# Kernel tuning notes

Measured on AMD Instinct MI355X. Metric: run time of the kernel, lower is better.

The kernel has to match this reference:

```python
import jax, jax.numpy as jnp
import numpy as np

jax.config.update("jax_enable_x64", True)

N_USERS = 100000
N_ITEMS = 50000
N = N_USERS + N_ITEMS          # total nodes
E = 4_000_000                  # nnz of adj
MASK_DEPTH = 2
KEEP_RATE = 0.1
N_SEEDS = 500


def setup_inputs() -> dict:
    key = jax.random.key(0)
    k1, k2, k3, k4 = jax.random.split(key, 4)
    rows = jax.random.randint(k1, (E,), 0, N, dtype=jnp.int64)
    cols = jax.random.randint(k2, (E,), 0, N, dtype=jnp.int64)
    seeds = jax.random.randint(k3, (N_SEEDS,), 0, N, dtype=jnp.int64)
    adj_vals = jax.random.uniform(k4, (E,), dtype=jnp.float32)
    return {"adj_vals": adj_vals, "rows": rows, "cols": cols, "seeds": seeds}


def _mask_subgraphs(adj_vals, rows, cols, seeds, key):
    # --- vectorized BFS-style edge masking (equivalent to the serial per-seed
    # loop: the set of removed edges per depth is the union over the frontier,
    # and collected endpoints are identical to the sequential version) ---
    alive = jnp.ones(E, dtype=bool)                    # edges not yet masked
    frontier = jnp.zeros(N, dtype=bool).at[seeds].set(True)
    masked_nodes = frontier                            # maskNodes accumulator
    for i in range(MASK_DEPTH):
        idct = (frontier[rows] | frontier[cols]) & alive
        alive = alive & ~idct
        if i != MASK_DEPTH - 1:
            hits = (jnp.zeros(N, jnp.int32)
                    .at[rows].add(idct.astype(jnp.int32))
                    .at[cols].add(idct.astype(jnp.int32)))
            frontier = hits > 0                        # unique(concat(nxtSeeds))
            masked_nodes = masked_nodes | frontier
    # random augmentation of the masked node set
    samp_num = int(N * KEEP_RATE)
    ks, kr, kc = jax.random.split(key, 3)
    sampled = jax.random.randint(ks, (samp_num,), 0, N)
    masked_nodes = masked_nodes.at[sampled].set(True)

    # --- encoderAdj: remaining edges with value 1, symmetric degree norm ---
    alive_f = alive.astype(jnp.float32)
    deg = jnp.zeros(N, jnp.float32).at[rows].add(alive_f)   # sparse row sum
    dnorm = jnp.power(deg + 1e-12, -0.5)
    enc_vals = alive_f * dnorm[rows] * dnorm[cols]          # 0 for masked edges

    # --- decoderAdj: random edges among masked nodes + self loops + remaining
    # edges, dedup'd through the row*N+col hash ---
    order = jnp.argsort(~masked_nodes)        # masked node ids first, ascending
    tem_num = masked_nodes.sum()
    i1 = jnp.minimum((jax.random.uniform(kr, (E,)) * tem_num).astype(jnp.int64),
                     tem_num - 1)
    i2 = jnp.minimum((jax.random.uniform(kc, (E,)) * tem_num).astype(jnp.int64),
                     tem_num - 1)
    tr = order[i1]
    tc = order[i2]
    ar = jnp.arange(N, dtype=jnp.int64)
    # masked (dead) edges collapse onto the (0,0) self-loop hash so the
    # fixed-size unique removes them, mirroring the compaction in torch
    h_tail = jnp.where(alive, rows * N + cols, 0)
    hashv = jnp.concatenate([tr * N + tc, tc * N + tr, ar * (N + 1), h_tail])
    uniq = jnp.unique(hashv, size=hashv.shape[0], fill_value=-1)
    valid = uniq >= 0
    dec_vals = valid.astype(jnp.float32)
    dec_cols = jnp.where(valid, uniq % N, 0)
    dec_rows = jnp.where(valid, uniq // N, 0)
    return rows, cols, enc_vals, dec_rows, dec_cols, dec_vals


def reference(adj_vals, rows, cols, seeds):
    key = jax.random.key(42)
    # returns (encoder indices+values, decoder indices+values); padded decoder
    # slots carry value 0 (equivalent sparse matrix)
    return _mask_subgraphs(adj_vals, rows, cols, seeds, key)
```

## Files before the change

### kernel.cpp

```cpp
#include <hip/hip_runtime.h>
#include <stdint.h>

#define NNODE   150000
#define EDGES   4000000
#define NSEED   500
#define NSAMP   15000
#define MOUT    12150000
#define SENTK   0xFFFFFFFFFFFFFFFFULL
#define SPAN    150000ULL
#define MULTK   51616ULL
#define FIXED   8150000

#define CHUNK   8192
#define TH      512
#define NC      1488
#define NCX     (NC / 8)
#define MP      ((size_t)NC * CHUNK)
#define RADIX   512
#define NHIST   (RADIX * NC)
#define SCB     (NHIST / 2048)
#define NTILE   NC

#define EBLK    2048
#define ENB     ((EDGES + EBLK - 1) / EBLK)

#define MTILE   2048
#define MB      ((NNODE + MTILE - 1) / MTILE)

#define OUT_DR  12000000
#define OUT_DC  24150000
#define OUT_DV  36300000

__host__ __device__ inline void tf2x32(uint32_t k0, uint32_t k1,
                                       uint32_t x0, uint32_t x1,
                                       uint32_t& o0, uint32_t& o1) {
  uint32_t ks2 = k0 ^ k1 ^ 0x1BD11BDAu;
  x0 += k0; x1 += k1;
#define TFR(d) { x0 += x1; x1 = (x1 << d) | (x1 >> (32 - d)); x1 ^= x0; }
  TFR(13) TFR(15) TFR(26) TFR(6)
  x0 += k1; x1 += ks2 + 1u;
  TFR(17) TFR(29) TFR(16) TFR(24)
  x0 += ks2; x1 += k0 + 2u;
  TFR(13) TFR(15) TFR(26) TFR(6)
  x0 += k0; x1 += k1 + 3u;
  TFR(17) TFR(29) TFR(16) TFR(24)
  x0 += k1; x1 += ks2 + 4u;
  TFR(13) TFR(15) TFR(26) TFR(6)
  x0 += ks2; x1 += k0 + 5u;
#undef TFR
  o0 = x0; o1 = x1;
}

__device__ inline unsigned long long tf_bits64(uint32_t k0, uint32_t k1, uint32_t i) {
  uint32_t o0, o1;
  tf2x32(k0, k1, 0u, i, o0, o1);
  return ((unsigned long long)o0 << 32) | o1;
}

__device__ inline int activeChunks(const int* counters) {
  int m2 = FIXED + counters[2];
  return (m2 + CHUNK - 1) / CHUNK;
}

__device__ inline int block_excl_scan_256(int v, int* lds , int& total) {
  int lane = threadIdx.x & 63, wid = threadIdx.x >> 6;
  int inc = v;
#pragma unroll
  for (int off = 1; off < 64; off <<= 1) {
    int y = __shfl_up(inc, off, 64);
    if (lane >= off) inc += y;
  }
  if (lane == 63) lds[wid] = inc;
  __syncthreads();
  if (threadIdx.x == 0) {
    int a = 0;
#pragma unroll
    for (int w = 0; w < 4; ++w) { int t = lds[w]; lds[w] = a; a += t; }
    lds[4] = a;
  }
  __syncthreads();
  total = lds[4];
  int res = inc - v + lds[wid];
  __syncthreads();
  return res;
}

__device__ inline void scan512_x4(const int v[4], int ex[4], int tot[4], int* aux) {
  int lane = threadIdx.x & 63, wid = threadIdx.x >> 6;
  int inc[4];
#pragma unroll
  for (int j = 0; j < 4; ++j) inc[j] = v[j];
#pragma unroll
  for (int off = 1; off < 64; off <<= 1) {
#pragma unroll
    for (int j = 0; j < 4; ++j) {
      int y = __shfl_up(inc[j], off, 64);
      if (lane >= off) inc[j] += y;
    }
  }
  if (lane == 63) {
#pragma unroll
    for (int j = 0; j < 4; ++j) aux[j * 8 + wid] = inc[j];
  }
  __syncthreads();
  if (threadIdx.x == 0) {
#pragma unroll
    for (int j = 0; j < 4; ++j) {
      int a = 0;
#pragma unroll
      for (int w = 0; w < 8; ++w) { int t = aux[j * 8 + w]; aux[j * 8 + w] = a; a += t; }
      aux[32 + j] = a;
    }
  }
  __syncthreads();
#pragma unroll
  for (int j = 0; j < 4; ++j) {
    ex[j] = inc[j] - v[j] + aux[j * 8 + wid];
    tot[j] = aux[32 + j];
  }
}

__device__ inline int scan512_1(int v, int* aux ) {
  int lane = threadIdx.x & 63, wid = threadIdx.x >> 6;
  int inc = v;
#pragma unroll
  for (int off = 1; off < 64; off <<= 1) {
    int y = __shfl_up(inc, off, 64);
    if (lane >= off) inc += y;
  }
  if (lane == 63) aux[wid] = inc;
  __syncthreads();
  if (threadIdx.x == 0) {
    int a = 0;
#pragma unroll
    for (int w = 0; w < 8; ++w) { int t = aux[w]; aux[w] = a; a += t; }
  }
  __syncthreads();
  return inc - v + aux[wid];
}

__device__ inline int phys16(int p) { return (p & ~15) | ((p + (p >> 4)) & 15); }

__global__ __launch_bounds__(256) void k_seed(const int* seeds, uint8_t* frontier, uint8_t* masked) {
  int i = blockIdx.x * 256 + threadIdx.x;
  if (i < NSEED) { int v = seeds[i]; frontier[v] = 1; masked[v] = 1; }
}

__global__ __launch_bounds__(256) void k_bfs0(const int* rows, const int* cols,
                                              const uint8_t* frontier, uint8_t* alive, uint8_t* nxt,
                                              float* out) {
  int e = blockIdx.x * 256 + threadIdx.x;
  int r = rows[e], c = cols[e];
  out[e] = (float)r;
  out[EDGES + e] = (float)c;
  if (frontier[r] | frontier[c]) { alive[e] = 0; nxt[r] = 1; nxt[c] = 1; }
}

__global__ __launch_bounds__(256) void k_masked_or(uint8_t* masked, const uint8_t* nxt) {
  int v = blockIdx.x * 256 + threadIdx.x;
  if (v < NNODE) masked[v] |= nxt[v];
}

__global__ __launch_bounds__(256) void k_bfs1deg(const int* rows, const int* cols,
                                                 const uint8_t* nxt, uint8_t* alive, float* deg) {
  int e = blockIdx.x * 256 + threadIdx.x;
  int r = rows[e];
  int a = alive[e];
  if (a && (nxt[r] | nxt[cols[e]])) { alive[e] = 0; a = 0; }
  if (a) atomicAdd(&deg[r], 1.0f);
}

__global__ __launch_bounds__(256) void k_sample(uint8_t* masked,
                                                uint32_t a0, uint32_t a1, uint32_t b0, uint32_t b1) {
  int i = blockIdx.x * 256 + threadIdx.x;
  if (i >= NSAMP) return;
  unsigned long long hi = tf_bits64(a0, a1, (uint32_t)i);
  unsigned long long lo = tf_bits64(b0, b1, (uint32_t)i);
  unsigned long long off = ((hi % SPAN) * MULTK + (lo % SPAN)) % SPAN;
  masked[off] = 1;
}

__global__ __launch_bounds__(256) void k_dnorm(const float* deg, float* dnorm) {
  int v = blockIdx.x * 256 + threadIdx.x;
  if (v < NNODE) {
    float x = deg[v] + 1e-12f;
    dnorm[v] = (float)(1.0 / sqrt((double)x));
  }
}

__global__ __launch_bounds__(256) void k_enctail(const int* rows, const int* cols,
                                                 const uint8_t* alive, const float* dnorm,
                                                 float* out, unsigned long long* A, int* counters) {
  __shared__ int lds[8];
  __shared__ unsigned long long stage[EBLK];
  __shared__ int sbase;
  int base = blockIdx.x * EBLK;
  unsigned long long vv[8];
  int emit[8], c = 0;
#pragma unroll
  for (int k = 0; k < 8; ++k) {
    int e = base + k * 256 + threadIdx.x;
    emit[k] = 0;
    if (e < EDGES) {
      int r = rows[e], cc = cols[e];
      int a = alive[e];
      out[2 * EDGES + e] = a ? dnorm[r] * dnorm[cc] : 0.0f;
      unsigned long long v = (unsigned long long)((long long)r * 150000LL + cc);
      if (a && v) { emit[k] = 1; vv[k] = v; c++; }
    }
  }
  int total;
  int ex = block_excl_scan_256(c, lds, total);
#pragma unroll
  for (int k = 0; k < 8; ++k) {
    if (emit[k]) stage[ex++] = vv[k];
  }
  if (threadIdx.x == 0) sbase = total ? atomicAdd(&counters[2], total) : 0;
  __syncthreads();
  int sb = sbase;
  for (int i = threadIdx.x; i < total; i += 256)
    A[(size_t)FIXED + sb + i] = stage[i];
}

__global__ __launch_bounds__(256) void k_mreduce(const uint8_t* masked, int* mPart) {
  __shared__ int lds[4];
  int base = blockIdx.x * MTILE;
  int s = 0;
  for (int i = threadIdx.x; i < MTILE; i += 256) {
    int idx = base + i;
    if (idx < NNODE) s += masked[idx];
  }
#pragma unroll
  for (int off = 32; off; off >>= 1) s += __shfl_down(s, off, 64);
  if ((threadIdx.x & 63) == 0) lds[threadIdx.x >> 6] = s;
  __syncthreads();
  if (threadIdx.x == 0) mPart[blockIdx.x] = lds[0] + lds[1] + lds[2] + lds[3];
}

__global__ __launch_bounds__(1024) void k_scan_small(int* part, int m, int* totalOut) {
  __shared__ int a[2048];
  int tid = threadIdx.x;
  a[tid] = (tid < m) ? part[tid] : 0;
  a[tid + 1024] = (tid + 1024 < m) ? part[tid + 1024] : 0;
  __syncthreads();
  for (int off = 1; off < 2048; off <<= 1) {
    int v1 = 0, v2;
    if (tid >= off) v1 = a[tid - off];
    v2 = a[tid + 1024 - off];
    __syncthreads();
    if (tid >= off) a[tid] += v1;
    a[tid + 1024] += v2;
    __syncthreads();
  }
  if (tid < m) part[tid] = (tid == 0) ? 0 : a[tid - 1];
  if (tid + 1024 < m) part[tid + 1024] = a[tid + 1023];
  if (tid == 0 && totalOut) *totalOut = a[2047];
}

__global__ __launch_bounds__(256) void k_mscatter(const uint8_t* masked, const int* mPart, int* mlist) {
  __shared__ int lds[8];
  int t0 = blockIdx.x * MTILE + threadIdx.x * 8;
  int c = 0;
#pragma unroll
  for (int k = 0; k < 8; ++k) { int idx = t0 + k; c += (idx < NNODE) ? masked[idx] : 0; }
  int total;
  int ex = block_excl_scan_256(c, lds, total);
  int run = mPart[blockIdx.x] + ex;
#pragma unroll
  for (int k = 0; k < 8; ++k) {
    int idx = t0 + k;
    if (idx < NNODE && masked[idx]) mlist[run++] = idx;
  }
}

__global__ __launch_bounds__(256) void k_build_pairs(const int* mlist, const int* counters,
                                                     unsigned long long* A,
                                                     uint32_t r0, uint32_t r1, uint32_t c0, uint32_t c1) {
  int e = blockIdx.x * 256 + threadIdx.x;
  long long tem = counters[1];
  unsigned long long bits = tf_bits64(r0, r1, (uint32_t)e);
  double u1 = __longlong_as_double((long long)((bits >> 12) | 0x3FF0000000000000ULL)) - 1.0;
  long long i1 = (long long)(u1 * (double)tem); if (i1 > tem - 1) i1 = tem - 1;
  bits = tf_bits64(c0, c1, (uint32_t)e);
  double u2 = __longlong_as_double((long long)((bits >> 12) | 0x3FF0000000000000ULL)) - 1.0;
  long long i2 = (long long)(u2 * (double)tem); if (i2 > tem - 1) i2 = tem - 1;
  long long tr = mlist[i1], tc = mlist[i2];
  A[2 * (size_t)e]     = (unsigned long long)(tr * 150000LL + tc);
  A[2 * (size_t)e + 1] = (unsigned long long)(tc * 150000LL + tr);
}

__global__ __launch_bounds__(256) void k_build_self(unsigned long long* A) {
  int v = blockIdx.x * 256 + threadIdx.x;
  if (v >= NNODE) return;
  A[2 * (size_t)EDGES + v] = (unsigned long long)v * 150001ULL;
}

__global__ __launch_bounds__(256) void k_pad(unsigned long long* A, const int* counters) {
  int m2 = FIXED + counters[2];
  int ac = (m2 + CHUNK - 1) / CHUNK;
  size_t idx = (size_t)m2 + blockIdx.x * 256 + threadIdx.x;
  if (idx < (size_t)ac * CHUNK) A[idx] = SENTK;
}

__global__ __launch_bounds__(TH) void k_rhist2(const unsigned long long* __restrict__ src,
                                               int* __restrict__ hist, int shift,
                                               const int* counters) {
  __shared__ int h8[RADIX * 4];
  int tid = threadIdx.x;
  int ac = activeChunks(counters);
  if ((int)blockIdx.x >= ac) { hist[(size_t)tid * NC + blockIdx.x] = 0; return; }
  for (int i = tid; i < RADIX * 4; i += TH) h8[i] = 0;
  __syncthreads();
  const ulonglong2* s2 = (const ulonglong2*)(src + (size_t)blockIdx.x * CHUNK);
  int rep = tid & 3, scnt = 0;
#pragma unroll
  for (int r = 0; r < 8; ++r) {
    ulonglong2 v = s2[tid + r * TH];
    int d0 = (int)((v.x >> shift) & (RADIX - 1));
    int d1 = (int)((v.y >> shift) & (RADIX - 1));
    if (d0 == RADIX - 1) scnt++; else atomicAdd(&h8[d0 * 4 + rep], 1);
    if (d1 == RADIX - 1) scnt++; else atomicAdd(&h8[d1 * 4 + rep], 1);
  }
  if (scnt) atomicAdd(&h8[(RADIX - 1) * 4 + rep], scnt);
  __syncthreads();
  int4 hv = *(const int4*)&h8[tid * 4];
  hist[(size_t)tid * NC + blockIdx.x] = hv.x + hv.y + hv.z + hv.w;
}

__global__ __launch_bounds__(256) void k_scan_reduce(const int* g, int* part, int n) {
  __shared__ int lds[4];
  int base = blockIdx.x * 2048;
  int s = 0;
  for (int i = threadIdx.x; i < 2048; i += 256) {
    int idx = base + i;
    if (idx < n) s += g[idx];
  }
#pragma unroll
  for (int off = 32; off; off >>= 1) s += __shfl_down(s, off, 64);
  if ((threadIdx.x & 63) == 0) lds[threadIdx.x >> 6] = s;
  __syncthreads();
  if (threadIdx.x == 0) part[blockIdx.x] = lds[0] + lds[1] + lds[2] + lds[3];
}

__global__ __launch_bounds__(256) void k_scan_apply(int* g, const int* part, int n) {
  __shared__ int lds[8];
  int t0 = blockIdx.x * 2048 + threadIdx.x * 8;
  int x[8];
#pragma unroll
  for (int k = 0; k < 8; ++k) { int idx = t0 + k; x[k] = (idx < n) ? g[idx] : 0; }
  int s = 0;
#pragma unroll
  for (int k = 0; k < 8; ++k) { int t = x[k]; x[k] = s; s += t; }
  int total;
  int ex = block_excl_scan_256(s, lds, total);
  int add = part[blockIdx.x] + ex;
#pragma unroll
  for (int k = 0; k < 8; ++k) { int idx = t0 + k; if (idx < n) g[idx] = x[k] + add; }
}

__global__ __launch_bounds__(TH) void k_rscatter2(const unsigned long long* __restrict__ src,
                                                  unsigned long long* __restrict__ dst,
                                                  const int* __restrict__ hist, int shift,
                                                  const int* counters) {
  __shared__ uint32_t klo[CHUNK], khi[CHUNK];
  __shared__ int h8[RADIX * 4];
  __shared__ int dstart[RADIX], gbase[RADIX];
  __shared__ int aux[40];
  int tid = threadIdx.x;
  int chunk = (blockIdx.x & 7) * NCX + (blockIdx.x >> 3);
  int ac = activeChunks(counters);
  if (chunk >= ac) return;
  size_t cbase = (size_t)chunk * CHUNK;
  gbase[tid] = hist[(size_t)tid * NC + chunk];
  for (int i = tid; i < RADIX * 4; i += TH) h8[i] = 0;
  __syncthreads();
  int rep = tid & 3;
  const ulonglong2* s2 = (const ulonglong2*)(src + cbase);
  int scnt = 0;
#pragma unroll
  for (int r = 0; r < 8; ++r) {
    ulonglong2 v = s2[tid + r * TH];
    int i = 2 * (tid + r * TH);
    int p0 = phys16(i), p1 = phys16(i + 1);
    klo[p0] = (uint32_t)v.x; khi[p0] = (uint32_t)(v.x >> 32);
    klo[p1] = (uint32_t)v.y; khi[p1] = (uint32_t)(v.y >> 32);
    int d0 = (int)((v.x >> shift) & (RADIX - 1));
    int d1 = (int)((v.y >> shift) & (RADIX - 1));
    if (d0 == RADIX - 1) scnt++; else atomicAdd(&h8[d0 * 4 + rep], 1);
    if (d1 == RADIX - 1) scnt++; else atomicAdd(&h8[d1 * 4 + rep], 1);
  }
  if (scnt) atomicAdd(&h8[(RADIX - 1) * 4 + rep], scnt);
  __syncthreads();
  int4 hv = *(const int4*)&h8[tid * 4];
  int h = hv.x + hv.y + hv.z + hv.w;
  int ex0 = scan512_1(h, aux);
  dstart[tid] = ex0;
  __syncthreads();
  int t0 = tid * 16;
  for (int rr = 0; rr < 3; ++rr) {
    int sh = shift + 3 * rr;
    unsigned long long key[16];
    unsigned long long cpack = 0;
#pragma unroll
    for (int k = 0; k < 16; ++k) {
      int p = phys16(t0 + k);
      key[k] = ((unsigned long long)khi[p] << 32) | klo[p];
      cpack += 1ULL << (((int)(key[k] >> sh) & 7) << 3);
    }
    int v4[4], ex[4], tot[4];
#pragma unroll
    for (int j = 0; j < 4; ++j) {
      unsigned pair = (unsigned)(cpack >> (16 * j));
      v4[j] = (int)((pair & 0xffu) | ((pair & 0xff00u) << 8));
    }
    scan512_x4(v4, ex, tot, aux);
    unsigned long long startq0, startq1;
    {
      int a = 0, s8[8];
#pragma unroll
      for (int j = 0; j < 4; ++j) {
        int tlo = tot[j] & 0xffff, thi = tot[j] >> 16;
        int elo = ex[j] & 0xffff,  ehi = ex[j] >> 16;
        s8[2 * j]     = a + elo; a += tlo;
        s8[2 * j + 1] = a + ehi; a += thi;
      }
      startq0 = (unsigned long long)(unsigned)s8[0]
              | ((unsigned long long)(unsigned)s8[1] << 16)
              | ((unsigned long long)(unsigned)s8[2] << 32)
              | ((unsigned long long)(unsigned)s8[3] << 48);
      startq1 = (unsigned long long)(unsigned)s8[4]
              | ((unsigned long long)(unsigned)s8[5] << 16)
              | ((unsigned long long)(unsigned)s8[6] << 32)
              | ((unsigned long long)(unsigned)s8[7] << 48);
    }
#pragma unroll
    for (int k = 0; k < 16; ++k) {
      int d = (int)(key[k] >> sh) & 7;
      int fs = (d & 3) << 4;
      unsigned long long inc = 1ULL << fs;
      int pos;
      if (d < 4) { pos = (int)((startq0 >> fs) & 0xffffu); startq0 += inc; }
      else       { pos = (int)((startq1 >> fs) & 0xffffu); startq1 += inc; }
      int p = phys16(pos);
      klo[p] = (uint32_t)key[k]; khi[p] = (uint32_t)(key[k] >> 32);
    }
    __syncthreads();
  }
#pragma unroll
  for (int r = 0; r < 16; ++r) {
    int i = tid + r * TH;
    int p = phys16(i);
    unsigned long long k1 = ((unsigned long long)khi[p] << 32) | klo[p];
    int d = (int)((k1 >> shift) & (RADIX - 1));
    dst[(size_t)(gbase[d] + (i - dstart[d]))] = k1;
  }
}

__global__ __launch_bounds__(TH) void k_uniq_count(const unsigned long long* A, int* uPart,
                                                   const int* counters) {
  __shared__ int lds[8];
  int ac = activeChunks(counters);
  if ((int)blockIdx.x >= ac) { if (threadIdx.x == 0) uPart[blockIdx.x] = 0; return; }
  size_t base = (size_t)blockIdx.x * CHUNK + (size_t)threadIdx.x * 16;
  unsigned long long prev = (base == 0) ? 0ULL : A[base - 1];
  int c = 0;
#pragma unroll
  for (int k = 0; k < 16; ++k) {
    unsigned long long v = A[base + k];
    c += (v != SENTK && v != prev) ? 1 : 0;
    prev = v;
  }
#pragma unroll
  for (int off = 32; off; off >>= 1) c += __shfl_down(c, off, 64);
  if ((threadIdx.x & 63) == 0) lds[threadIdx.x >> 6] = c;
  __syncthreads();
  if (threadIdx.x == 0) {
    int s = 0;
#pragma unroll
    for (int w = 0; w < 8; ++w) s += lds[w];
    uPart[blockIdx.x] = s;
  }
}

__global__ __launch_bounds__(TH) void k_final(const unsigned long long* A, const int* uPart,
                                              const int* counters, float* out) {
  __shared__ int aux[9];
  __shared__ float sq[CHUNK], sr[CHUNK];
  __shared__ int scnt;
  int ac = activeChunks(counters);
  if ((int)blockIdx.x >= ac) return;
  size_t base = (size_t)blockIdx.x * CHUNK + (size_t)threadIdx.x * 16;
  unsigned long long v[16];
  int f[16], c = 0;
  unsigned long long prev = (base == 0) ? 0ULL : A[base - 1];
#pragma unroll
  for (int k = 0; k < 16; ++k) {
    v[k] = A[base + k];
    f[k] = (v[k] != SENTK && v[k] != prev) ? 1 : 0;
    c += f[k];
    prev = v[k];
  }
  int ex = scan512_1(c, aux);
  if (threadIdx.x == TH - 1) scnt = ex + c;
  int j = ex;
#pragma unroll
  for (int k = 0; k < 16; ++k) {
    if (f[k]) {
      unsigned long long val = v[k];
      long long q = (long long)((double)val * (1.0 / 150000.0));
      long long r = (long long)val - q * 150000LL;
      if (r < 0) { q--; r += 150000LL; }
      else if (r >= 150000LL) { q++; r -= 150000LL; }
      sq[j] = (float)q; sr[j] = (float)r; j++;
    }
  }
  __syncthreads();
  int cnt = scnt;
  int jb = 1 + uPart[blockIdx.x];
  for (int i = (int)threadIdx.x; i < cnt; i += TH) {
    out[OUT_DR + jb + i] = sq[i];
    out[OUT_DC + jb + i] = sr[i];
  }
}

__global__ __launch_bounds__(256) void k_dectail(const int* counters, float* out) {
  int i = (blockIdx.x * 256 + threadIdx.x) * 4;
  if (i >= MOUT) return;
  int totU = counters[3] + 1;
  float4 dv;
  dv.x = (i + 0 < totU) ? 1.0f : 0.0f;
  dv.y = (i + 1 < totU) ? 1.0f : 0.0f;
  dv.z = (i + 2 < totU) ? 1.0f : 0.0f;
  dv.w = (i + 3 < totU) ? 1.0f : 0.0f;
  *(float4*)&out[OUT_DV + i] = dv;
  if (i + 3 >= totU) {
    float4 z = make_float4(0.0f, 0.0f, 0.0f, 0.0f);
    if (i >= totU) {
      *(float4*)&out[OUT_DR + i] = z;
      *(float4*)&out[OUT_DC + i] = z;
    } else {
#pragma unroll
      for (int k = 0; k < 4; ++k)
        if (i + k >= totU) { out[OUT_DR + i + k] = 0.0f; out[OUT_DC + i + k] = 0.0f; }
    }
  }
  if (i == 0) { out[OUT_DR] = 0.0f; out[OUT_DC] = 0.0f; }
}

extern "C" void kernel_launch(void* const* d_in, const int* in_sizes, int n_in,
                              void* d_out, int out_size, void* d_ws, size_t ws_size,
                              hipStream_t stream) {
  const int* rows = (const int*)d_in[1];
  const int* cols = (const int*)d_in[2];
  const int* seeds = (const int*)d_in[3];
  float* out = (float*)d_out;

  char* ws = (char*)d_ws;
  size_t off = 0;
  auto alloc = [&](size_t bytes) -> char* {
    char* p = ws + off;
    off += (bytes + 255) & ~(size_t)255;
    return p;
  };
  unsigned long long* A = (unsigned long long*)alloc(MP * 8);
  uint8_t* alive = (uint8_t*)alloc(EDGES);
  char* zbase = ws + off;
  uint8_t* frontier = (uint8_t*)alloc(NNODE);
  uint8_t* nextf = (uint8_t*)alloc(NNODE);
  uint8_t* masked = (uint8_t*)alloc(NNODE);
  float* deg = (float*)alloc((size_t)NNODE * 4);
  int* counters = (int*)alloc(256 * 4);
  size_t zsize = (size_t)((ws + off) - zbase);
  float* dnorm = (float*)alloc((size_t)NNODE * 4);
  int* mlist = (int*)alloc((size_t)NNODE * 4);
  int* hist = (int*)alloc((size_t)NHIST * 4);
  int* spart = (int*)alloc(2048 * 4);
  int* uPart = (int*)alloc(2048 * 4);
  int* mPart = (int*)alloc(256 * 4);

  unsigned long long* Bbuf = (unsigned long long*)(out + OUT_DR);

  uint32_t ks0, ks1, kr0, kr1, kc0, kc1, s10, s11, s20, s21;
  tf2x32(0u, 42u, 0u, 0u, ks0, ks1);
  tf2x32(0u, 42u, 0u, 1u, kr0, kr1);
  tf2x32(0u, 42u, 0u, 2u, kc0, kc1);
  tf2x32(ks0, ks1, 0u, 0u, s10, s11);
  tf2x32(ks0, ks1, 0u, 1u, s20, s21);

  hipMemsetAsync(zbase, 0, zsize, stream);
  hipMemsetAsync(alive, 1, EDGES, stream);

  const int EB = EDGES / 256;
  const int NB = (NNODE + 255) / 256;

  k_seed<<<2, 256, 0, stream>>>(seeds, frontier, masked);
  k_bfs0<<<EB, 256, 0, stream>>>(rows, cols, frontier, alive, nextf, out);
  k_masked_or<<<NB, 256, 0, stream>>>(masked, nextf);
  k_bfs1deg<<<EB, 256, 0, stream>>>(rows, cols, nextf, alive, deg);
  k_sample<<<(NSAMP + 255) / 256, 256, 0, stream>>>(masked, s10, s11, s20, s21);
  k_dnorm<<<NB, 256, 0, stream>>>(deg, dnorm);
  k_enctail<<<ENB, 256, 0, stream>>>(rows, cols, alive, dnorm, out, A, counters);

  k_mreduce<<<MB, 256, 0, stream>>>(masked, mPart);
  k_scan_small<<<1, 1024, 0, stream>>>(mPart, MB, counters + 1);
  k_mscatter<<<MB, 256, 0, stream>>>(masked, mPart, mlist);

  k_build_pairs<<<EB, 256, 0, stream>>>(mlist, counters, A, kr0, kr1, kc0, kc1);
  k_build_self<<<NB, 256, 0, stream>>>(A);
  k_pad<<<CHUNK / 256, 256, 0, stream>>>(A, counters);

  unsigned long long* src = A;
  unsigned long long* dst = Bbuf;
  const int shifts[4] = {0, 9, 18, 27};
  for (int p = 0; p < 4; ++p) {
    k_rhist2<<<NC, TH, 0, stream>>>(src, hist, shifts[p], counters);
    k_scan_reduce<<<SCB, 256, 0, stream>>>(hist, spart, NHIST);
    k_scan_small<<<1, 1024, 0, stream>>>(spart, SCB, nullptr);
    k_scan_apply<<<SCB, 256, 0, stream>>>(hist, spart, NHIST);
    k_rscatter2<<<NC, TH, 0, stream>>>(src, dst, hist, shifts[p], counters);
    unsigned long long* t = src; src = dst; dst = t;
  }

  k_uniq_count<<<NTILE, TH, 0, stream>>>(src, uPart, counters);
  k_scan_small<<<1, 1024, 0, stream>>>(uPart, NTILE, counters + 3);
  k_final<<<NTILE, TH, 0, stream>>>(src, uPart, counters, out);
  k_dectail<<<(MOUT / 4 + 255) / 256, 256, 0, stream>>>(counters, out);
}
```

Before: 1.049 ms.

## Vectorize BFS edge kernels, privatize degree atomics, store radix keys as 64-bit LDS

The two BFS edge passes now handle four edges per thread with int4 and uchar4 vector loads and stores. k_bfs0 writes every alive byte directly, which removes the memset of alive. Degree counting uses integer atomics spread over eight private copies selected by block index, and k_dnorm sums the copies. This is meant to reduce atomic contention and memory traffic. The radix scatter stores keys as single 64-bit LDS words instead of split lo/hi arrays, which changes the LDS bank access pattern and risks bank conflicts.

```diff
diff --git a/kernel.cpp b/kernel.cpp
--- a/kernel.cpp
+++ b/kernel.cpp
@@ -2,6 +2,7 @@
 #include <stdint.h>
 
 #define NNODE   150000
+#define NNODE16 150016
 #define EDGES   4000000
 #define NSEED   500
 #define NSAMP   15000
@@ -23,6 +24,8 @@
 
 #define EBLK    2048
 #define ENB     ((EDGES + EBLK - 1) / EBLK)
+
+#define VNB     ((EDGES + 1023) / 1024)
 
 #define MTILE   2048
 #define MB      ((NNODE + MTILE - 1) / MTILE)
@@ -149,11 +152,33 @@
 __global__ __launch_bounds__(256) void k_bfs0(const int* rows, const int* cols,
                                               const uint8_t* frontier, uint8_t* alive, uint8_t* nxt,
                                               float* out) {
-  int e = blockIdx.x * 256 + threadIdx.x;
-  int r = rows[e], c = cols[e];
-  out[e] = (float)r;
-  out[EDGES + e] = (float)c;
-  if (frontier[r] | frontier[c]) { alive[e] = 0; nxt[r] = 1; nxt[c] = 1; }
+  int g = blockIdx.x * 1024 + threadIdx.x * 4;
+  if (g >= EDGES) return;
+  if (g + 4 <= EDGES) {
+    int4 r4 = *(const int4*)&rows[g];
+    int4 c4 = *(const int4*)&cols[g];
+    int rr[4] = {r4.x, r4.y, r4.z, r4.w};
+    int cc[4] = {c4.x, c4.y, c4.z, c4.w};
+    *(float4*)&out[g] = make_float4((float)rr[0], (float)rr[1], (float)rr[2], (float)rr[3]);
+    *(float4*)&out[EDGES + g] = make_float4((float)cc[0], (float)cc[1], (float)cc[2], (float)cc[3]);
+    uint8_t al[4];
+#pragma unroll
+    for (int k = 0; k < 4; ++k) {
+      int hit = frontier[rr[k]] | frontier[cc[k]];
+      al[k] = (uint8_t)(1 - hit);
+      if (hit) { nxt[rr[k]] = 1; nxt[cc[k]] = 1; }
+    }
+    *(uchar4*)&alive[g] = make_uchar4(al[0], al[1], al[2], al[3]);
+  } else {
+    for (int e = g; e < EDGES; ++e) {
+      int r = rows[e], c = cols[e];
+      out[e] = (float)r;
+      out[EDGES + e] = (float)c;
+      int hit = frontier[r] | frontier[c];
+      alive[e] = (uint8_t)(1 - hit);
+      if (hit) { nxt[r] = 1; nxt[c] = 1; }
+    }
+  }
 }
 
 __global__ __launch_bounds__(256) void k_masked_or(uint8_t* masked, const uint8_t* nxt) {
@@ -162,12 +187,36 @@
 }
 
 __global__ __launch_bounds__(256) void k_bfs1deg(const int* rows, const int* cols,
-                                                 const uint8_t* nxt, uint8_t* alive, float* deg) {
-  int e = blockIdx.x * 256 + threadIdx.x;
-  int r = rows[e];
-  int a = alive[e];
-  if (a && (nxt[r] | nxt[cols[e]])) { alive[e] = 0; a = 0; }
-  if (a) atomicAdd(&deg[r], 1.0f);
+                                                 const uint8_t* nxt, uint8_t* alive, int* deg8) {
+  int g = blockIdx.x * 1024 + threadIdx.x * 4;
+  if (g >= EDGES) return;
+  int* dmy = deg8 + (blockIdx.x & 7) * NNODE16;
+  if (g + 4 <= EDGES) {
+    int4 r4 = *(const int4*)&rows[g];
+    int4 c4 = *(const int4*)&cols[g];
+    uchar4 a4 = *(const uchar4*)&alive[g];
+    int rr[4] = {r4.x, r4.y, r4.z, r4.w};
+    int cc[4] = {c4.x, c4.y, c4.z, c4.w};
+    uint8_t aa[4] = {a4.x, a4.y, a4.z, a4.w};
+    uint8_t na[4];
+#pragma unroll
+    for (int k = 0; k < 4; ++k) {
+      int a = aa[k];
+      if (a && (nxt[rr[k]] | nxt[cc[k]])) a = 0;
+      na[k] = (uint8_t)a;
+    }
+    *(uchar4*)&alive[g] = make_uchar4(na[0], na[1], na[2], na[3]);
+#pragma unroll
+    for (int k = 0; k < 4; ++k)
+      if (na[k]) atomicAdd(&dmy[rr[k]], 1);
+  } else {
+    for (int e = g; e < EDGES; ++e) {
+      int a = alive[e];
+      int r = rows[e];
+      if (a && (nxt[r] | nxt[cols[e]])) { alive[e] = 0; a = 0; }
+      if (a) atomicAdd(&dmy[r], 1);
+    }
+  }
 }
 
 __global__ __launch_bounds__(256) void k_sample(uint8_t* masked,
@@ -180,10 +229,13 @@
   masked[off] = 1;
 }
 
-__global__ __launch_bounds__(256) void k_dnorm(const float* deg, float* dnorm) {
+__global__ __launch_bounds__(256) void k_dnorm(const int* deg8, float* dnorm) {
   int v = blockIdx.x * 256 + threadIdx.x;
   if (v < NNODE) {
-    float x = deg[v] + 1e-12f;
+    int s = 0;
+#pragma unroll
+    for (int j = 0; j < 8; ++j) s += deg8[j * NNODE16 + v];
+    float x = (float)s + 1e-12f;
     dnorm[v] = (float)(1.0 / sqrt((double)x));
   }
 }
@@ -362,7 +414,7 @@
                                                   unsigned long long* __restrict__ dst,
                                                   const int* __restrict__ hist, int shift,
                                                   const int* counters) {
-  __shared__ uint32_t klo[CHUNK], khi[CHUNK];
+  __shared__ unsigned long long kk[CHUNK];
   __shared__ int h8[RADIX * 4];
   __shared__ int dstart[RADIX], gbase[RADIX];
   __shared__ int aux[40];
@@ -381,9 +433,8 @@
   for (int r = 0; r < 8; ++r) {
     ulonglong2 v = s2[tid + r * TH];
     int i = 2 * (tid + r * TH);
-    int p0 = phys16(i), p1 = phys16(i + 1);
-    klo[p0] = (uint32_t)v.x; khi[p0] = (uint32_t)(v.x >> 32);
-    klo[p1] = (uint32_t)v.y; khi[p1] = (uint32_t)(v.y >> 32);
+    kk[phys16(i)] = v.x;
+    kk[phys16(i + 1)] = v.y;
     int d0 = (int)((v.x >> shift) & (RADIX - 1));
     int d1 = (int)((v.y >> shift) & (RADIX - 1));
     if (d0 == RADIX - 1) scnt++; else atomicAdd(&h8[d0 * 4 + rep], 1);
@@ -403,8 +454,7 @@
     unsigned long long cpack = 0;
 #pragma unroll
     for (int k = 0; k < 16; ++k) {
-      int p = phys16(t0 + k);
-      key[k] = ((unsigned long long)khi[p] << 32) | klo[p];
+      key[k] = kk[phys16(t0 + k)];
       cpack += 1ULL << (((int)(key[k] >> sh) & 7) << 3);
     }
     int v4[4], ex[4], tot[4];
@@ -441,16 +491,14 @@
       int pos;
       if (d < 4) { pos = (int)((startq0 >> fs) & 0xffffu); startq0 += inc; }
       else       { pos = (int)((startq1 >> fs) & 0xffffu); startq1 += inc; }
-      int p = phys16(pos);
-      klo[p] = (uint32_t)key[k]; khi[p] = (uint32_t)(key[k] >> 32);
+      kk[phys16(pos)] = key[k];
     }
     __syncthreads();
   }
 #pragma unroll
   for (int r = 0; r < 16; ++r) {
     int i = tid + r * TH;
-    int p = phys16(i);
-    unsigned long long k1 = ((unsigned long long)khi[p] << 32) | klo[p];
+    unsigned long long k1 = kk[phys16(i)];
     int d = (int)((k1 >> shift) & (RADIX - 1));
     dst[(size_t)(gbase[d] + (i - dstart[d]))] = k1;
   }
@@ -568,7 +616,7 @@
   uint8_t* frontier = (uint8_t*)alloc(NNODE);
   uint8_t* nextf = (uint8_t*)alloc(NNODE);
   uint8_t* masked = (uint8_t*)alloc(NNODE);
-  float* deg = (float*)alloc((size_t)NNODE * 4);
+  int* deg8 = (int*)alloc((size_t)8 * NNODE16 * 4);
   int* counters = (int*)alloc(256 * 4);
   size_t zsize = (size_t)((ws + off) - zbase);
   float* dnorm = (float*)alloc((size_t)NNODE * 4);
@@ -588,17 +636,16 @@
   tf2x32(ks0, ks1, 0u, 1u, s20, s21);
 
   hipMemsetAsync(zbase, 0, zsize, stream);
-  hipMemsetAsync(alive, 1, EDGES, stream);
 
   const int EB = EDGES / 256;
   const int NB = (NNODE + 255) / 256;
 
   k_seed<<<2, 256, 0, stream>>>(seeds, frontier, masked);
-  k_bfs0<<<EB, 256, 0, stream>>>(rows, cols, frontier, alive, nextf, out);
+  k_bfs0<<<VNB, 256, 0, stream>>>(rows, cols, frontier, alive, nextf, out);
   k_masked_or<<<NB, 256, 0, stream>>>(masked, nextf);
-  k_bfs1deg<<<EB, 256, 0, stream>>>(rows, cols, nextf, alive, deg);
+  k_bfs1deg<<<VNB, 256, 0, stream>>>(rows, cols, nextf, alive, deg8);
   k_sample<<<(NSAMP + 255) / 256, 256, 0, stream>>>(masked, s10, s11, s20, s21);
-  k_dnorm<<<NB, 256, 0, stream>>>(deg, dnorm);
+  k_dnorm<<<NB, 256, 0, stream>>>(deg8, dnorm);
   k_enctail<<<ENB, 256, 0, stream>>>(rows, cols, alive, dnorm, out, A, counters);
 
   k_mreduce<<<MB, 256, 0, stream>>>(masked, mPart);
```

After: 1.001 ms. 1.05x faster.
